# Optimization experiments

Measured on AMD Instinct MI355X. Metric: run time of the kernel, lower is better.

The kernel has to match this reference:

```python
import jax, jax.numpy as jnp
import numpy as np

POINT_DIM, VOXEL_DIM, NUM_HEADS = 3, 256, 8
HEAD_DIM = VOXEL_DIM // NUM_HEADS


def _linear_params(key, fan_in, fan_out):
    kw, kb = jax.random.split(key)
    bound = 1.0 / np.sqrt(fan_in)
    W = jax.random.uniform(kw, (fan_out, fan_in), jnp.float32, -bound, bound)
    b = jax.random.uniform(kb, (fan_out,), jnp.float32, -bound, bound)
    return W, b


def setup_inputs() -> dict:
    key = jax.random.key(0)
    ks = jax.random.split(key, 7)
    points = jax.random.normal(ks[0], (2, 4096, POINT_DIM), jnp.float32)
    voxel_features = jax.random.normal(ks[1], (2, 2048, VOXEL_DIM), jnp.float32)
    Wp, bp = _linear_params(ks[2], POINT_DIM, VOXEL_DIM)
    Wq, bq = _linear_params(ks[3], VOXEL_DIM, VOXEL_DIM)
    Wk, bk = _linear_params(ks[4], VOXEL_DIM, VOXEL_DIM)
    Wv, bv = _linear_params(ks[5], VOXEL_DIM, VOXEL_DIM)
    Wf, bf = _linear_params(ks[6], VOXEL_DIM * 2, VOXEL_DIM)
    return {
        "points": points, "voxel_features": voxel_features,
        "Wp": Wp, "bp": bp, "Wq": Wq, "bq": bq,
        "Wk": Wk, "bk": bk, "Wv": Wv, "bv": bv,
        "Wf": Wf, "bf": bf,
    }


def reference(points, voxel_features, Wp, bp, Wq, bq, Wk, bk, Wv, bv, Wf, bf):
    B, N, _ = points.shape
    M = voxel_features.shape[1]
    # projections (torch Linear: x @ W.T + b)
    point_features = points @ Wp.T + bp                      # [B,N,D]
    q = (point_features @ Wq.T + bq).reshape(B, N, NUM_HEADS, HEAD_DIM)
    k = (voxel_features @ Wk.T + bk).reshape(B, M, NUM_HEADS, HEAD_DIM)
    v = (voxel_features @ Wv.T + bv).reshape(B, M, NUM_HEADS, HEAD_DIM)
    # attention scores [B,H,N,M]
    scale = 1.0 / np.sqrt(HEAD_DIM).astype(np.float32)
    attn = jnp.einsum('bnhd,bmhd->bhnm', q, k) * scale
    attn = jax.nn.softmax(attn, axis=-1)
    attended = jnp.einsum('bhnm,bmhd->bnhd', attn, v).reshape(B, N, VOXEL_DIM)
    fused = jnp.concatenate([point_features, attended], axis=-1) @ Wf.T + bf
    return fused
```

## Files before the change

### kernel.cpp

```cpp
#include <hip/hip_runtime.h>

#define B_ 2
#define N_ 4096
#define M_ 2048
#define D_ 256
#define H_ 8
#define DH_ 32
#define ROWS_ (B_*N_)
#define KVROWS_ (B_*M_)
#define PRE_ (0.17677669529663687f * 1.4426950408889634f)
#define CBASE_ 32.0f

typedef __attribute__((ext_vector_type(8))) short short8_t;
typedef __attribute__((ext_vector_type(4))) float float4_t;

#if defined(__has_builtin)
# if __has_builtin(__builtin_amdgcn_exp2f)
#  define EXP2F(x) __builtin_amdgcn_exp2f(x)
# else
#  define EXP2F(x) exp2f(x)
# endif
#else
# define EXP2F(x) exp2f(x)
#endif

__device__ __forceinline__ unsigned int rne_u(float f) {
    union { float f; unsigned int u; } c;
    c.f = f;
    return c.u + 0x7FFFu + ((c.u >> 16) & 1u);
}

__device__ __forceinline__ unsigned short f2us(float f) {
    return (unsigned short)(rne_u(f) >> 16);
}

__device__ __forceinline__ unsigned int pack2rn(float a, float b) {
    return __builtin_amdgcn_perm(rne_u(b), rne_u(a), 0x07060302u);
}

__device__ __forceinline__ unsigned int pack2tr(float a, float b) {
    union { float f; unsigned int u; } x, y;
    x.f = a; y.f = b;
    return __builtin_amdgcn_perm(y.u, x.u, 0x07060302u);
}

__device__ __forceinline__ short8_t cvt8(float4 a, float4 b) {
    union { unsigned int u[4]; short8_t s; } c;
    c.u[0] = pack2rn(a.x, a.y);
    c.u[1] = pack2rn(a.z, a.w);
    c.u[2] = pack2rn(b.x, b.y);
    c.u[3] = pack2rn(b.z, b.w);
    return c.s;
}

__device__ __forceinline__ int xcd_swz(int bid, int nwg) {
    const int cpx = nwg >> 3;
    return (bid & 7) * cpx + (bid >> 3);
}

template<int K, int NCOL, int LDSRC>
__device__ __forceinline__ void stageB2(const float* __restrict__ W, int col0, int kof,
                                        unsigned short* __restrict__ Bs, int tid)
{
    const int n = tid & (NCOL - 1), g = tid / NCOL;
    const int GROUPS = 256 / NCOL;
    const int CPT = (K / 8) / GROUPS;
    const float* src = W + (size_t)(col0 + n) * LDSRC + kof + g * (K / GROUPS);
#pragma unroll
    for (int ci = 0; ci < CPT; ci++) {
        int logc = g * CPT + ci;
        int phys = logc ^ (n & 7);
        short8_t v = cvt8(*(const float4*)(src + ci * 8), *(const float4*)(src + ci * 8 + 4));
        *(short8_t*)(Bs + (size_t)n * K + phys * 8) = v;
    }
}

template<int K>
__device__ __forceinline__ short8_t readB(const unsigned short* __restrict__ Bs,
                                          int c, int l16, int quad, int k0)
{
    int phys = ((k0 >> 3) + quad) ^ (l16 & 7);
    return *(const short8_t*)(Bs + (size_t)(16 * c + l16) * K + phys * 8);
}

__global__ __launch_bounds__(256) void g_projkv(
    const float* __restrict__ voxel,
    const float* __restrict__ Wp, const float* __restrict__ bp,
    const float* __restrict__ Wq, const float* __restrict__ bq,
    const float* __restrict__ Wk, const float* __restrict__ bk,
    const float* __restrict__ Wv, const float* __restrict__ bv,
    const float* __restrict__ Wf, const float* __restrict__ bfb,
    unsigned short* __restrict__ k_g, unsigned short* __restrict__ vt_g,
    float* __restrict__ Wqc, float* __restrict__ Wfc)
{
    const int tid = threadIdx.x;
    const int wave = tid >> 6, lane = tid & 63, quad = lane >> 4, l16 = lane & 15;

    __shared__ unsigned short Bs[64 * 256];
    __shared__ unsigned short Bs2[64 * 256];

    if (blockIdx.x < 256) {
        const int bid = (int)blockIdx.x;
        const int row0 = (bid >> 2) * 64;
        const int col0 = (bid & 3) * 64;
        const float* arow = voxel + (size_t)(row0 + wave * 16 + l16) * D_;

        stageB2<256, 64, 256>(Wk, col0, 0, Bs, tid);
        stageB2<256, 64, 256>(Wv, col0, 0, Bs2, tid);

        float4_t ak[4], av[4];
#pragma unroll
        for (int c = 0; c < 4; c++) {
            ak[c] = (float4_t){0.f, 0.f, 0.f, 0.f};
            av[c] = (float4_t){0.f, 0.f, 0.f, 0.f};
        }
        __syncthreads();
#pragma unroll
        for (int k0 = 0; k0 < 256; k0 += 32) {
            short8_t af = cvt8(*(const float4*)(arow + k0 + quad * 8),
                               *(const float4*)(arow + k0 + quad * 8 + 4));
#pragma unroll
            for (int c = 0; c < 4; c++) {
                ak[c] = __builtin_amdgcn_mfma_f32_16x16x32_bf16(af, readB<256>(Bs,  c, l16, quad, k0), ak[c], 0, 0, 0);
                av[c] = __builtin_amdgcn_mfma_f32_16x16x32_bf16(af, readB<256>(Bs2, c, l16, quad, k0), av[c], 0, 0, 0);
            }
        }
        const int b = row0 / M_;
        const int m0 = row0 - b * M_ + wave * 16 + quad * 4;
#pragma unroll
        for (int c = 0; c < 4; c++) {
            int col = col0 + 16 * c + l16;
            float bbk = bk[col], bbv = bv[col];
#pragma unroll
            for (int r = 0; r < 4; r++) {
                int row = row0 + wave * 16 + quad * 4 + r;
                k_g[(size_t)row * D_ + col] = f2us(ak[c][r] + bbk);
            }
            int h = col >> 5, dh = col & 31;
            unsigned int u0 = pack2rn(av[c][0] + bbv, av[c][1] + bbv);
            unsigned int u1 = pack2rn(av[c][2] + bbv, av[c][3] + bbv);
            *(uint2*)(vt_g + (size_t)((b * H_ + h) * DH_ + dh) * M_ + m0) = make_uint2(u0, u1);
        }
    } else {
        const int role = (int)blockIdx.x - 256;
        float* wps = (float*)Bs;
        *(float4*)(wps + tid * 4) = make_float4(Wp[tid * 3 + 0], Wp[tid * 3 + 1],
                                                Wp[tid * 3 + 2], bp[tid]);
        __syncthreads();
        const int col = tid;
        const float* wrow = role ? (Wf + (size_t)col * 512) : (Wq + (size_t)col * 256);
        float a0 = 0.f, a1 = 0.f, a2 = 0.f, ab = 0.f;
#pragma unroll 4
        for (int d = 0; d < 256; d += 4) {
            float4 wv = *(const float4*)(wrow + d);
            float4 w0 = *(const float4*)(wps + (d + 0) * 4);
            float4 w1 = *(const float4*)(wps + (d + 1) * 4);
            float4 w2 = *(const float4*)(wps + (d + 2) * 4);
            float4 w3 = *(const float4*)(wps + (d + 3) * 4);
            a0 += wv.x * w0.x + wv.y * w1.x + wv.z * w2.x + wv.w * w3.x;
            a1 += wv.x * w0.y + wv.y * w1.y + wv.z * w2.y + wv.w * w3.y;
            a2 += wv.x * w0.z + wv.y * w1.z + wv.z * w2.z + wv.w * w3.z;
            ab += wv.x * w0.w + wv.y * w1.w + wv.z * w2.w + wv.w * w3.w;
        }
        if (role == 0) {
            *(float4*)(Wqc + (size_t)col * 4) =
                make_float4(a0 * PRE_, a1 * PRE_, a2 * PRE_, (ab + bq[col]) * PRE_);
        } else {
            *(float4*)(Wfc + (size_t)col * 4) =
                make_float4(a0, a1, a2, ab + bfb[col]);
        }
    }
}

__global__ __launch_bounds__(256) void k_attn7(
    const float* __restrict__ points, const float* __restrict__ Wqc,
    const unsigned short* __restrict__ k_g,
    const unsigned short* __restrict__ vt_g,
    unsigned short* __restrict__ att_g)
{
    const int tid = threadIdx.x;
    const int w = tid >> 6, lane = tid & 63, quad = lane >> 4, l16 = lane & 15;
    const int lbid = xcd_swz((int)blockIdx.x, B_ * H_ * (N_ / 64));
    const int nt = lbid & 63;
    const int bh = lbid >> 6;
    const int b = bh >> 3, h = bh & 7;
    const int n0 = nt * 64 + w * 16;

    __shared__ unsigned short Kt[2][64][40];
    __shared__ unsigned short Vt[2][32][72];
    __shared__ unsigned short Pb[4][16][64];

    const unsigned short* kbase = k_g + (size_t)(b * M_) * D_ + h * DH_;
    const unsigned short* vbase = vt_g + (size_t)(bh * DH_) * M_;

    const int kr = tid >> 2, kc = tid & 3;
    const int vr = tid >> 3, vc = tid & 7;

    *(short8_t*)&Kt[0][kr][kc * 8] = *(const short8_t*)(kbase + (size_t)kr * D_ + kc * 8);
    *(short8_t*)&Vt[0][vr][vc * 8] = *(const short8_t*)(vbase + (size_t)vr * M_ + vc * 8);

    const size_t qrow = (size_t)(b * N_ + n0 + l16);
    const float p0 = points[qrow * 3 + 0];
    const float p1 = points[qrow * 3 + 1];
    const float p2 = points[qrow * 3 + 2];
    float q8[8];
#pragma unroll
    for (int j = 0; j < 8; j++) {
        float4 wc = *(const float4*)(Wqc + (size_t)(h * DH_ + quad * 8 + j) * 4);
        q8[j] = p0 * wc.x + p1 * wc.y + p2 * wc.z + wc.w;
    }
    short8_t qf = cvt8(make_float4(q8[0], q8[1], q8[2], q8[3]),
                       make_float4(q8[4], q8[5], q8[6], q8[7]));

    float4_t od0 = {0.f, 0.f, 0.f, 0.f};
    float4_t od1 = {0.f, 0.f, 0.f, 0.f};
    float l_lane = 0.f;

    unsigned short* pb = &Pb[w][0][0];
    const int h7 = l16 & 7;
    const float4_t zc = {-CBASE_, -CBASE_, -CBASE_, -CBASE_};

    for (int s = 0; s < M_ / 64; s++) {
        __syncthreads();
        const int buf = s & 1;
        const bool more = (s + 1 < M_ / 64);
        short8_t knext, vnext;
        if (more) {
            const int kv1 = (s + 1) * 64;
            knext = *(const short8_t*)(kbase + (size_t)(kv1 + kr) * D_ + kc * 8);
            vnext = *(const short8_t*)(vbase + (size_t)vr * M_ + kv1 + vc * 8);
        }

        float4_t st[4];
        __builtin_amdgcn_s_setprio(1);
#pragma unroll
        for (int t = 0; t < 4; t++) {
            short8_t kf = *(const short8_t*)&Kt[buf][16 * t + l16][quad * 8];
            st[t] = __builtin_amdgcn_mfma_f32_16x16x32_bf16(kf, qf, zc, 0, 0, 0);
        }
        __builtin_amdgcn_s_setprio(0);

        float psum = 0.f;
#pragma unroll
        for (int t = 0; t < 4; t++) {
            float p0e = EXP2F(st[t][0]);
            float p1e = EXP2F(st[t][1]);
            float p2e = EXP2F(st[t][2]);
            float p3e = EXP2F(st[t][3]);
            psum += (p0e + p1e) + (p2e + p3e);
            unsigned int u0 = pack2tr(p0e, p1e);
            unsigned int u1 = pack2tr(p2e, p3e);
            int phys = (2 * t + (quad >> 1)) ^ h7;
            *(uint2*)(pb + l16 * 64 + phys * 8 + (quad & 1) * 4) = make_uint2(u0, u1);
        }
        l_lane += psum;

        short8_t pfa = *(const short8_t*)(pb + l16 * 64 + (quad ^ h7) * 8);
        short8_t pfb = *(const short8_t*)(pb + l16 * 64 + ((4 + quad) ^ h7) * 8);

        short8_t vf00 = *(const short8_t*)&Vt[buf][l16][quad * 8];
        short8_t vf01 = *(const short8_t*)&Vt[buf][l16][32 + quad * 8];
        short8_t vf10 = *(const short8_t*)&Vt[buf][16 + l16][quad * 8];
        short8_t vf11 = *(const short8_t*)&Vt[buf][16 + l16][32 + quad * 8];
        __builtin_amdgcn_s_setprio(1);
        od0 = __builtin_amdgcn_mfma_f32_16x16x32_bf16(vf00, pfa, od0, 0, 0, 0);
        od0 = __builtin_amdgcn_mfma_f32_16x16x32_bf16(vf01, pfb, od0, 0, 0, 0);
        od1 = __builtin_amdgcn_mfma_f32_16x16x32_bf16(vf10, pfa, od1, 0, 0, 0);
        od1 = __builtin_amdgcn_mfma_f32_16x16x32_bf16(vf11, pfb, od1, 0, 0, 0);
        __builtin_amdgcn_s_setprio(0);

        if (more) {
            *(short8_t*)&Kt[buf ^ 1][kr][kc * 8] = knext;
            *(short8_t*)&Vt[buf ^ 1][vr][vc * 8] = vnext;
        }
    }

    l_lane += __shfl_xor(l_lane, 16);
    l_lane += __shfl_xor(l_lane, 32);
    const float inv = 1.0f / l_lane;

    unsigned short* ob = att_g + (size_t)(b * N_ + n0 + l16) * D_ + h * DH_;
    {
        unsigned int u0 = pack2rn(od0[0] * inv, od0[1] * inv);
        unsigned int u1 = pack2rn(od0[2] * inv, od0[3] * inv);
        *(uint2*)(ob + quad * 4) = make_uint2(u0, u1);
        unsigned int u2 = pack2rn(od1[0] * inv, od1[1] * inv);
        unsigned int u3 = pack2rn(od1[2] * inv, od1[3] * inv);
        *(uint2*)(ob + 16 + quad * 4) = make_uint2(u2, u3);
    }
}

__global__ __launch_bounds__(256) void g_fuse2(
    const unsigned short* __restrict__ att_g,
    const float* __restrict__ points, const float* __restrict__ Wfc,
    const float* __restrict__ Wf,
    float* __restrict__ out)
{
    const int tid = threadIdx.x;
    const int wave = tid >> 6, lane = tid & 63, quad = lane >> 4, l16 = lane & 15;
    const int lbid = xcd_swz((int)blockIdx.x, (ROWS_ / 64) * 8);
    const int row0 = (lbid >> 3) * 64;
    const int col0 = (lbid & 7) * 32;

    __shared__ unsigned short Bs[32 * 256];

    stageB2<256, 32, 512>(Wf, col0, 256, Bs, tid);
    __syncthreads();

    float4_t acc[2];
#pragma unroll
    for (int c = 0; c < 2; c++) acc[c] = (float4_t){0.f, 0.f, 0.f, 0.f};

    const size_t arow = (size_t)(row0 + wave * 16 + l16) * D_;
#pragma unroll
    for (int k0 = 0; k0 < 256; k0 += 32) {
        short8_t af = *(const short8_t*)(att_g + arow + k0 + quad * 8);
#pragma unroll
        for (int c = 0; c < 2; c++)
            acc[c] = __builtin_amdgcn_mfma_f32_16x16x32_bf16(af, readB<256>(Bs, c, l16, quad, k0), acc[c], 0, 0, 0);
    }

    const int rbase = row0 + wave * 16 + quad * 4;
    float px[4], py[4], pz[4];
#pragma unroll
    for (int r = 0; r < 4; r++) {
        px[r] = points[(size_t)(rbase + r) * 3 + 0];
        py[r] = points[(size_t)(rbase + r) * 3 + 1];
        pz[r] = points[(size_t)(rbase + r) * 3 + 2];
    }
#pragma unroll
    for (int c = 0; c < 2; c++) {
        int col = col0 + 16 * c + l16;
        float4 wf = *(const float4*)(Wfc + (size_t)col * 4);
#pragma unroll
        for (int r = 0; r < 4; r++) {
            out[(size_t)(rbase + r) * D_ + col] =
                acc[c][r] + px[r] * wf.x + py[r] * wf.y + pz[r] * wf.z + wf.w;
        }
    }
}

extern "C" void kernel_launch(void* const* d_in, const int* in_sizes, int n_in,
                              void* d_out, int out_size, void* d_ws, size_t ws_size,
                              hipStream_t stream)
{
    const float* points = (const float*)d_in[0];
    const float* voxel  = (const float*)d_in[1];
    const float* Wp  = (const float*)d_in[2];
    const float* bp  = (const float*)d_in[3];
    const float* Wq  = (const float*)d_in[4];
    const float* bq  = (const float*)d_in[5];
    const float* Wk  = (const float*)d_in[6];
    const float* bk  = (const float*)d_in[7];
    const float* Wv  = (const float*)d_in[8];
    const float* bv  = (const float*)d_in[9];
    const float* Wf  = (const float*)d_in[10];
    const float* bfb = (const float*)d_in[11];
    float* out = (float*)d_out;

    float* Wqc = (float*)d_ws;
    float* Wfc = Wqc + 256 * 4;
    unsigned short* k_g   = (unsigned short*)(Wfc + 256 * 4);
    unsigned short* vt_g  = k_g  + (size_t)KVROWS_ * D_;
    unsigned short* att_g = vt_g + (size_t)KVROWS_ * D_;

    g_projkv<<<dim3(258),  dim3(256), 0, stream>>>(voxel, Wp, bp, Wq, bq, Wk, bk,
                                                   Wv, bv, Wf, bfb, k_g, vt_g, Wqc, Wfc);
    k_attn7 <<<dim3(B_ * H_ * (N_ / 64)), dim3(256), 0, stream>>>(points, Wqc, k_g, vt_g, att_g);
    g_fuse2 <<<dim3((ROWS_ / 64) * 8), dim3(256), 0, stream>>>(att_g, points, Wfc, Wf, out);
}
```

Measured before the change: 143.4 us.

## Permute K rows so softmax probabilities feed PV MFMA directly from registers

Stores K tiles in shared memory with a row swizzle and reads them in a permuted order. The score MFMA output lanes then line up with the B-operand layout the PV MFMA expects, so the per-wave LDS round-trip for P (write, read back, Pb buffer) is removed. It also drops the s_setprio hints, unrolls the main loop by two, and advances the global K/V pointers incrementally. The risk is register pressure and a correctness dependence on the permutation matching the key order of the V tile.

```diff
diff --git a/kernel.cpp b/kernel.cpp
--- a/kernel.cpp
+++ b/kernel.cpp
@@ -172,7 +172,7 @@
     }
 }
 
-__global__ __launch_bounds__(256) void k_attn7(
+__global__ __launch_bounds__(256) void k_attn9(
     const float* __restrict__ points, const float* __restrict__ Wqc,
     const unsigned short* __restrict__ k_g,
     const unsigned short* __restrict__ vt_g,
@@ -188,16 +188,26 @@
 
     __shared__ unsigned short Kt[2][64][40];
     __shared__ unsigned short Vt[2][32][72];
-    __shared__ unsigned short Pb[4][16][64];
 
     const unsigned short* kbase = k_g + (size_t)(b * M_) * D_ + h * DH_;
     const unsigned short* vbase = vt_g + (size_t)(bh * DH_) * M_;
 
     const int kr = tid >> 2, kc = tid & 3;
     const int vr = tid >> 3, vc = tid & 7;
-
-    *(short8_t*)&Kt[0][kr][kc * 8] = *(const short8_t*)(kbase + (size_t)kr * D_ + kc * 8);
-    *(short8_t*)&Vt[0][vr][vc * 8] = *(const short8_t*)(vbase + (size_t)vr * M_ + vc * 8);
+    const int ksr = kr ^ ((kr & 8) >> 1);
+
+    const unsigned short* kq = kbase + (size_t)kr * D_ + kc * 8;
+    const unsigned short* vq = vbase + (size_t)vr * M_ + vc * 8;
+
+    *(short8_t*)&Kt[0][ksr][kc * 8] = *(const short8_t*)kq;
+    *(short8_t*)&Vt[0][vr][vc * 8] = *(const short8_t*)vq;
+
+    const int rbas = 8 * (l16 >> 2) + (l16 & 3);
+    const int rx = l16 & 4;
+    int krow[4];
+#pragma unroll
+    for (int t = 0; t < 4; t++)
+        krow[t] = (rbas + 4 * (t & 1) + 32 * (t >> 1)) ^ rx;
 
     const size_t qrow = (size_t)(b * N_ + n0 + l16);
     const float p0 = points[qrow * 3 + 0];
@@ -216,31 +226,30 @@
     float4_t od1 = {0.f, 0.f, 0.f, 0.f};
     float l_lane = 0.f;
 
-    unsigned short* pb = &Pb[w][0][0];
-    const int h7 = l16 & 7;
     const float4_t zc = {-CBASE_, -CBASE_, -CBASE_, -CBASE_};
 
+#pragma unroll 2
     for (int s = 0; s < M_ / 64; s++) {
         __syncthreads();
         const int buf = s & 1;
         const bool more = (s + 1 < M_ / 64);
         short8_t knext, vnext;
         if (more) {
-            const int kv1 = (s + 1) * 64;
-            knext = *(const short8_t*)(kbase + (size_t)(kv1 + kr) * D_ + kc * 8);
-            vnext = *(const short8_t*)(vbase + (size_t)vr * M_ + kv1 + vc * 8);
+            kq += 64 * D_;
+            vq += 64;
+            knext = *(const short8_t*)kq;
+            vnext = *(const short8_t*)vq;
         }
 
         float4_t st[4];
-        __builtin_amdgcn_s_setprio(1);
 #pragma unroll
         for (int t = 0; t < 4; t++) {
-            short8_t kf = *(const short8_t*)&Kt[buf][16 * t + l16][quad * 8];
+            short8_t kf = *(const short8_t*)&Kt[buf][krow[t]][quad * 8];
             st[t] = __builtin_amdgcn_mfma_f32_16x16x32_bf16(kf, qf, zc, 0, 0, 0);
         }
-        __builtin_amdgcn_s_setprio(0);
 
         float psum = 0.f;
+        unsigned int uu[4][2];
 #pragma unroll
         for (int t = 0; t < 4; t++) {
             float p0e = EXP2F(st[t][0]);
@@ -248,29 +257,26 @@
             float p2e = EXP2F(st[t][2]);
             float p3e = EXP2F(st[t][3]);
             psum += (p0e + p1e) + (p2e + p3e);
-            unsigned int u0 = pack2tr(p0e, p1e);
-            unsigned int u1 = pack2tr(p2e, p3e);
-            int phys = (2 * t + (quad >> 1)) ^ h7;
-            *(uint2*)(pb + l16 * 64 + phys * 8 + (quad & 1) * 4) = make_uint2(u0, u1);
+            uu[t][0] = pack2tr(p0e, p1e);
+            uu[t][1] = pack2tr(p2e, p3e);
         }
         l_lane += psum;
 
-        short8_t pfa = *(const short8_t*)(pb + l16 * 64 + (quad ^ h7) * 8);
-        short8_t pfb = *(const short8_t*)(pb + l16 * 64 + ((4 + quad) ^ h7) * 8);
+        union { unsigned int u[4]; short8_t s; } pa, pb2;
+        pa.u[0]  = uu[0][0]; pa.u[1]  = uu[0][1]; pa.u[2]  = uu[1][0]; pa.u[3]  = uu[1][1];
+        pb2.u[0] = uu[2][0]; pb2.u[1] = uu[2][1]; pb2.u[2] = uu[3][0]; pb2.u[3] = uu[3][1];
 
         short8_t vf00 = *(const short8_t*)&Vt[buf][l16][quad * 8];
         short8_t vf01 = *(const short8_t*)&Vt[buf][l16][32 + quad * 8];
         short8_t vf10 = *(const short8_t*)&Vt[buf][16 + l16][quad * 8];
         short8_t vf11 = *(const short8_t*)&Vt[buf][16 + l16][32 + quad * 8];
-        __builtin_amdgcn_s_setprio(1);
-        od0 = __builtin_amdgcn_mfma_f32_16x16x32_bf16(vf00, pfa, od0, 0, 0, 0);
-        od0 = __builtin_amdgcn_mfma_f32_16x16x32_bf16(vf01, pfb, od0, 0, 0, 0);
-        od1 = __builtin_amdgcn_mfma_f32_16x16x32_bf16(vf10, pfa, od1, 0, 0, 0);
-        od1 = __builtin_amdgcn_mfma_f32_16x16x32_bf16(vf11, pfb, od1, 0, 0, 0);
-        __builtin_amdgcn_s_setprio(0);
+        od0 = __builtin_amdgcn_mfma_f32_16x16x32_bf16(vf00, pa.s,  od0, 0, 0, 0);
+        od0 = __builtin_amdgcn_mfma_f32_16x16x32_bf16(vf01, pb2.s, od0, 0, 0, 0);
+        od1 = __builtin_amdgcn_mfma_f32_16x16x32_bf16(vf10, pa.s,  od1, 0, 0, 0);
+        od1 = __builtin_amdgcn_mfma_f32_16x16x32_bf16(vf11, pb2.s, od1, 0, 0, 0);
 
         if (more) {
-            *(short8_t*)&Kt[buf ^ 1][kr][kc * 8] = knext;
+            *(short8_t*)&Kt[buf ^ 1][ksr][kc * 8] = knext;
             *(short8_t*)&Vt[buf ^ 1][vr][vc * 8] = vnext;
         }
     }
@@ -366,6 +372,6 @@
 
     g_projkv<<<dim3(258),  dim3(256), 0, stream>>>(voxel, Wp, bp, Wq, bq, Wk, bk,
                                                    Wv, bv, Wf, bfb, k_g, vt_g, Wqc, Wfc);
-    k_attn7 <<<dim3(B_ * H_ * (N_ / 64)), dim3(256), 0, stream>>>(points, Wqc, k_g, vt_g, att_g);
+    k_attn9 <<<dim3(B_ * H_ * (N_ / 64)), dim3(256), 0, stream>>>(points, Wqc, k_g, vt_g, att_g);
     g_fuse2 <<<dim3((ROWS_ / 64) * 8), dim3(256), 0, stream>>>(att_g, points, Wfc, Wf, out);
 }
```

New measurement: 134.9 us. -5.9%, faster.
